# Optimization experiments

Measured on AMD Instinct MI355X. Metric: run time of the kernel, lower is better.

The kernel has to match this reference:

```python
import jax, jax.numpy as jnp
import numpy as np
from jax import lax

B, EMB, HEADS, HD, LAYERS, FIX, ADAPT, MLP, NCLS = 32, 768, 12, 64, 12, 6, 6, 3072, 100
PE_N, PE_D = 100, 256
SCALE = 1.0 / np.sqrt(HD)


def _ln(x, g, b, eps=1e-5):
    m = jnp.mean(x, axis=-1, keepdims=True)
    v = jnp.mean((x - m) ** 2, axis=-1, keepdims=True)
    return (x - m) / jnp.sqrt(v + eps) * g + b


def _vit_block(x, g1, b1, qkvw, qkvb, pw, pb, g2, b2, f1w, f1b, f2w, f2b):
    Bn, N, _ = x.shape
    h = _ln(x, g1, b1)
    qkv = (h @ qkvw + qkvb).reshape(Bn, N, 3, HEADS, HD)
    q, k, v = [qkv[:, :, i].transpose(0, 2, 1, 3) for i in range(3)]  # [B,H,N,hd]
    attn = jax.nn.softmax(jnp.einsum('bhqd,bhkd->bhqk', q, k) * SCALE, axis=-1)
    o = jnp.einsum('bhqk,bhkd->bhqd', attn, v).transpose(0, 2, 1, 3).reshape(Bn, N, EMB)
    x = x + (o @ pw + pb)
    h = _ln(x, g2, b2)
    return x + (jax.nn.gelu(h @ f1w + f1b, approximate=False) @ f2w + f2b)


def _sinusoid_table():
    pos = np.arange(PE_N)[:, None].astype(np.float64)
    j = np.arange(PE_D)[None, :]
    ang = pos / np.power(10000.0, 2 * (j // 2) / PE_D)
    tab = ang.copy()
    tab[:, 0::2] = np.sin(ang[:, 0::2])
    tab[:, 1::2] = np.cos(ang[:, 1::2])
    return jnp.asarray(tab, dtype=jnp.float32)


def setup_inputs() -> dict:
    key = jax.random.key(0)
    ks = iter(jax.random.split(key, 40))
    r = lambda shape: jax.random.normal(next(ks), shape, dtype=jnp.float32) * 0.02
    inp = {
        'x': jax.random.normal(next(ks), (B, 3, 224, 224), dtype=jnp.float32),
        'budget': jax.random.uniform(next(ks), (B,), dtype=jnp.float32),
        'pe_table': _sinusoid_table(),
        'lat_w1': r((PE_D, EMB)), 'lat_b1': r((EMB,)),
        'lat_ln_g': jnp.ones((EMB,), jnp.float32), 'lat_ln_b': jnp.zeros((EMB,), jnp.float32),
        'lat_w2': r((EMB, EMB)), 'lat_b2': r((EMB,)),
        'patch_w': r((EMB, 3, 16, 16)), 'patch_b': r((EMB,)),
        'cls_token': r((1, 1, EMB)), 'pos_embed': r((1, 198, EMB)),
        'sched_w': r((EMB, ADAPT)), 'sched_b': r((ADAPT,)),
        'ln1_g': jnp.ones((LAYERS, EMB), jnp.float32), 'ln1_b': jnp.zeros((LAYERS, EMB), jnp.float32),
        'qkv_w': r((LAYERS, EMB, 3 * EMB)), 'qkv_b': r((LAYERS, 3 * EMB)),
        'proj_w': r((LAYERS, EMB, EMB)), 'proj_b': r((LAYERS, EMB)),
        'ln2_g': jnp.ones((LAYERS, EMB), jnp.float32), 'ln2_b': jnp.zeros((LAYERS, EMB), jnp.float32),
        'fc1_w': r((LAYERS, EMB, MLP)), 'fc1_b': r((LAYERS, MLP)),
        'fc2_w': r((LAYERS, MLP, EMB)), 'fc2_b': r((LAYERS, EMB)),
        'norm_g': jnp.ones((EMB,), jnp.float32), 'norm_b': jnp.zeros((EMB,), jnp.float32),
        'head_w': r((EMB, NCLS)), 'head_b': r((NCLS,)),
    }
    return inp


def reference(x, budget, pe_table, lat_w1, lat_b1, lat_ln_g, lat_ln_b, lat_w2, lat_b2,
              patch_w, patch_b, cls_token, pos_embed, sched_w, sched_b,
              ln1_g, ln1_b, qkv_w, qkv_b, proj_w, proj_b, ln2_g, ln2_b,
              fc1_w, fc1_b, fc2_w, fc2_b, norm_g, norm_b, head_w, head_b):
    Bn = x.shape[0]
    bud = lax.stop_gradient(budget)
    # latency encoder
    idx = jnp.round(bud * (PE_N - 1)).astype(jnp.int32)
    h = pe_table[idx] @ lat_w1 + lat_b1
    h = jax.nn.gelu(h, approximate=False)
    h = _ln(h, lat_ln_g, lat_ln_b)
    lat = (h @ lat_w2 + lat_b2)[:, None, :]  # [B,1,EMB]
    # patch embed: conv16 s16 -> [B,EMB,14,14]
    p = lax.conv_general_dilated(x, patch_w, (16, 16), 'VALID',
                                 dimension_numbers=('NCHW', 'OIHW', 'NCHW'))
    p = (p + patch_b[None, :, None, None]).reshape(Bn, EMB, 196).transpose(0, 2, 1)
    tok = jnp.concatenate([lat, jnp.broadcast_to(cls_token, (Bn, 1, EMB)), p], axis=1)
    tok = tok + pos_embed  # [B,198,EMB]
    blk = lambda t, i: _vit_block(t, ln1_g[i], ln1_b[i], qkv_w[i], qkv_b[i], proj_w[i], proj_b[i],
                                  ln2_g[i], ln2_b[i], fc1_w[i], fc1_b[i], fc2_w[i], fc2_b[i])
    for i in range(FIX):
        tok = blk(tok, i)
    # layer routing (eval path): per-sample top-k over adaptive layers
    logits = tok[:, 0] @ sched_w + sched_b  # [B,ADAPT]
    k = jnp.maximum(jnp.ceil(bud * ADAPT).astype(jnp.int32), 1)  # [B]
    ranks = jnp.argsort(jnp.argsort(-logits, axis=-1), axis=-1)
    active = ranks < k[:, None]  # [B,ADAPT] bool
    t = tok[:, 1:]  # drop latency token -> [B,197,EMB]
    for i in range(ADAPT):
        out = blk(t, FIX + i)
        t = jnp.where(active[:, i, None, None], out, t)
    t = _ln(t, norm_g, norm_b)
    return t[:, 0] @ head_w + head_b
```

## Files before the change

kernel.cpp:

```cpp
#include <hip/hip_runtime.h>
#include <hip/hip_bf16.h>
#include <math.h>


using bf16   = __hip_bfloat16;
using short8 = __attribute__((ext_vector_type(8))) short;
using f32x4  = __attribute__((ext_vector_type(4))) float;

#define GLD16(gptr, lptr)                                                            \
    __builtin_amdgcn_global_load_lds((const __attribute__((address_space(1))) void*)(gptr), \
                                     (__attribute__((address_space(3))) void*)(lptr), 16, 0, 0)

__device__ __forceinline__ void split2(float x, short& h, short& l)
{
    unsigned u  = __float_as_uint(x);
    unsigned hr = (u + 0x7fffu + ((u >> 16) & 1u)) & 0xffff0000u;
    h = (short)(hr >> 16);
    float res = x - __uint_as_float(hr);
    l = (short)(__float_as_uint(res) >> 16);
}

__global__ __launch_bounds__(256) void trans_split_kernel(const float* __restrict__ W,
                                                          short* __restrict__ Wh,
                                                          short* __restrict__ Wl,
                                                          int K, int N)
{
    __shared__ float tile[32][33];
    int n0 = blockIdx.x * 32, k0 = blockIdx.y * 32;
    int c = threadIdx.x & 31, r = threadIdx.x >> 5;
    #pragma unroll
    for (int i = 0; i < 32; i += 8)
        tile[r + i][c] = W[(size_t)(k0 + r + i) * N + n0 + c];
    __syncthreads();
    #pragma unroll
    for (int i = 0; i < 32; i += 8) {
        short h, l; split2(tile[c][r + i], h, l);
        size_t o = (size_t)(n0 + r + i) * K + k0 + c;
        Wh[o] = h; Wl[o] = l;
    }
}

__global__ void split_kernel(const float* __restrict__ in, short* __restrict__ h,
                             short* __restrict__ l, int n)
{
    int i = blockIdx.x * 256 + threadIdx.x;
    if (i >= n) return;
    short hh, ll; split2(in[i], hh, ll);
    h[i] = hh; l[i] = ll;
}

__global__ void im2col_split_kernel(const float* __restrict__ x,
                                    short* __restrict__ Ah, short* __restrict__ Al)
{
    int idx = blockIdx.x * 256 + threadIdx.x;
    if (idx >= 6272 * 768) return;
    int k = idx % 768;
    int row = idx / 768;
    int b = row / 196, p = row % 196;
    int py = p / 14, px = p % 14;
    int c = k >> 8, rem = k & 255;
    int i = rem >> 4, j = rem & 15;
    float v = x[(((size_t)b * 3 + c) * 224 + py * 16 + i) * 224 + px * 16 + j];
    short h, l; split2(v, h, l);
    Ah[idx] = h; Al[idx] = l;
}

template<bool GELU, bool RES, bool SPLITOUT>
__global__ __launch_bounds__(256) void gemm3_kernel(const short* __restrict__ Ah,
                                                    const short* __restrict__ Al,
                                                    const short* __restrict__ Bh,
                                                    const short* __restrict__ Bl,
                                                    const float* __restrict__ bias,
                                                    const float* __restrict__ resid,
                                                    float* __restrict__ Cf,
                                                    short* __restrict__ Ch,
                                                    short* __restrict__ Cl,
                                                    int M, int N, int K)
{
    __shared__ __align__(16) short sm[2 * 4 * 128 * 32];
    const int tid  = threadIdx.x;
    const int lane = tid & 63;
    const int w    = tid >> 6;
    const int wm   = w >> 1, wn = w & 1;
    const int m0   = blockIdx.y * 128;
    const int n0   = blockIdx.x * 128;
    const int col  = lane & 15;
    const int quad = lane >> 4;
    const int srow = lane >> 2;
    const int skc  = (((lane & 3) ^ ((lane >> 3) & 3)) * 8);
    const int rswz = (quad ^ ((col >> 1) & 3)) * 8;

    f32x4 acc[4][4];
    #pragma unroll
    for (int i = 0; i < 4; ++i)
        #pragma unroll
        for (int j = 0; j < 4; ++j) acc[i][j] = (f32x4)0.f;

    const short* Ahb = Ah + (size_t)m0 * K;
    const short* Alb = Al + (size_t)m0 * K;
    const short* Bhb = Bh + (size_t)n0 * K;
    const short* Blb = Bl + (size_t)n0 * K;

    auto stage = [&](int buf, int t) {
        const int k0 = t << 5;
        short* dst = &sm[buf * 16384];
        #pragma unroll
        for (int i = 0; i < 2; ++i) {
            int r = w * 32 + i * 16;
            size_t go = (size_t)(r + srow) * K + k0 + skc;
            GLD16(Ahb + go, dst + r * 32);
            GLD16(Alb + go, dst + 4096 + r * 32);
            GLD16(Bhb + go, dst + 8192 + r * 32);
            GLD16(Blb + go, dst + 12288 + r * 32);
        }
    };

    auto compute = [&](int buf) {
        const short* cb = &sm[buf * 16384];
        short8 ah[4], al[4];
        #pragma unroll
        for (int mi = 0; mi < 4; ++mi) {
            int ao = (wm * 64 + mi * 16 + col) * 32 + rswz;
            ah[mi] = *(const short8*)(cb + ao);
            al[mi] = *(const short8*)(cb + 4096 + ao);
        }
        #pragma unroll
        for (int ni = 0; ni < 4; ++ni) {
            int bo = (wn * 64 + ni * 16 + col) * 32 + rswz;
            short8 bh = *(const short8*)(cb + 8192 + bo);
            short8 bl = *(const short8*)(cb + 12288 + bo);
            #pragma unroll
            for (int mi = 0; mi < 4; ++mi) {
                acc[mi][ni] = __builtin_amdgcn_mfma_f32_16x16x32_bf16(ah[mi], bh, acc[mi][ni], 0, 0, 0);
                acc[mi][ni] = __builtin_amdgcn_mfma_f32_16x16x32_bf16(al[mi], bh, acc[mi][ni], 0, 0, 0);
                acc[mi][ni] = __builtin_amdgcn_mfma_f32_16x16x32_bf16(ah[mi], bl, acc[mi][ni], 0, 0, 0);
            }
        }
    };

    const int nk = K >> 5;
    stage(0, 0);
    __syncthreads();
    int cur = 0;
    for (int t = 0; t < nk - 1; ++t) {
        stage(cur ^ 1, t + 1);
        compute(cur);
        __syncthreads();
        cur ^= 1;
    }
    compute(cur);

    #pragma unroll
    for (int mi = 0; mi < 4; ++mi) {
        #pragma unroll
        for (int ni = 0; ni < 4; ++ni) {
            int gcol = n0 + wn * 64 + ni * 16 + col;
            float bv = bias[gcol];
            #pragma unroll
            for (int r = 0; r < 4; ++r) {
                int grow = m0 + wm * 64 + mi * 16 + quad * 4 + r;
                if (grow < M) {
                    float v = acc[mi][ni][r] + bv;
                    if (RES) v += resid[(size_t)grow * N + gcol];
                    if (GELU) v = 0.5f * v * (1.f + erff(v * 0.70710678118654752f));
                    size_t o = (size_t)grow * N + gcol;
                    if (SPLITOUT) { short h, l; split2(v, h, l); Ch[o] = h; Cl[o] = l; }
                    else          Cf[o] = v;
                }
            }
        }
    }
}

__global__ __launch_bounds__(256) void ln_kernel(const float* __restrict__ x,
                                                 const float* __restrict__ g,
                                                 const float* __restrict__ bta,
                                                 short* __restrict__ outh,
                                                 short* __restrict__ outl, int M)
{
    int row = blockIdx.x * 4 + (threadIdx.x >> 6);
    int lane = threadIdx.x & 63;
    if (row >= M) return;
    const float* xr = x + (size_t)row * 768;
    float vals[12];
    float s = 0.f;
    #pragma unroll
    for (int i = 0; i < 12; ++i) { vals[i] = xr[lane + i * 64]; s += vals[i]; }
    #pragma unroll
    for (int off = 32; off; off >>= 1) s += __shfl_xor(s, off);
    float mean = s * (1.f / 768.f);
    float vs = 0.f;
    #pragma unroll
    for (int i = 0; i < 12; ++i) { float d = vals[i] - mean; vs += d * d; }
    #pragma unroll
    for (int off = 32; off; off >>= 1) vs += __shfl_xor(vs, off);
    float rstd = rsqrtf(vs * (1.f / 768.f) + 1e-5f);
    size_t rb = (size_t)row * 768;
    #pragma unroll
    for (int i = 0; i < 12; ++i) {
        int c = lane + i * 64;
        short h, l; split2((vals[i] - mean) * rstd * g[c] + bta[c], h, l);
        outh[rb + c] = h; outl[rb + c] = l;
    }
}

__global__ __launch_bounds__(256) void attn_kernel(const float* __restrict__ qkv,
                                                   short* __restrict__ Oh,
                                                   short* __restrict__ Ol, int S)
{
    __shared__ float Ks[128 * 64];
    __shared__ float Vs[128 * 64];
    int bh = blockIdx.x;
    int b = bh / 12, h = bh % 12;
    const float* base = qkv + (size_t)b * S * 2304;
    int tid = threadIdx.x;
    int r = tid;
    bool act = (r < S);
    float q[64];
    #pragma unroll
    for (int d = 0; d < 64; ++d) q[d] = 0.f;
    if (act) {
        const float4* qp = (const float4*)(base + (size_t)r * 2304 + h * 64);
        #pragma unroll
        for (int d4 = 0; d4 < 16; ++d4) {
            float4 t = qp[d4];
            q[4 * d4] = t.x; q[4 * d4 + 1] = t.y; q[4 * d4 + 2] = t.z; q[4 * d4 + 3] = t.w;
        }
    }
    float o[64];
    #pragma unroll
    for (int d = 0; d < 64; ++d) o[d] = 0.f;
    float m = -1e30f, l = 0.f;

    for (int jc = 0; jc < S; jc += 128) {
        int cnt = min(128, S - jc);
        __syncthreads();
        for (int idx = tid; idx < cnt * 64; idx += 256) {
            int j = idx >> 6, d = idx & 63;
            const float* rp = base + (size_t)(jc + j) * 2304 + h * 64 + d;
            Ks[idx] = rp[768];
            Vs[idx] = rp[1536];
        }
        __syncthreads();
        if (act) {
            for (int j = 0; j < cnt; ++j) {
                const float4* kr = (const float4*)&Ks[j * 64];
                float s0 = 0.f, s1 = 0.f, s2 = 0.f, s3 = 0.f;
                #pragma unroll
                for (int d4 = 0; d4 < 16; ++d4) {
                    float4 kv = kr[d4];
                    s0 += q[4 * d4]     * kv.x;
                    s1 += q[4 * d4 + 1] * kv.y;
                    s2 += q[4 * d4 + 2] * kv.z;
                    s3 += q[4 * d4 + 3] * kv.w;
                }
                float s = ((s0 + s1) + (s2 + s3)) * 0.125f;
                float mn = fmaxf(m, s);
                float alpha = expf(m - mn);
                float p = expf(s - mn);
                l = l * alpha + p;
                m = mn;
                const float4* vr = (const float4*)&Vs[j * 64];
                #pragma unroll
                for (int d4 = 0; d4 < 16; ++d4) {
                    float4 vv = vr[d4];
                    o[4 * d4]     = o[4 * d4]     * alpha + p * vv.x;
                    o[4 * d4 + 1] = o[4 * d4 + 1] * alpha + p * vv.y;
                    o[4 * d4 + 2] = o[4 * d4 + 2] * alpha + p * vv.z;
                    o[4 * d4 + 3] = o[4 * d4 + 3] * alpha + p * vv.w;
                }
            }
        }
    }
    if (act) {
        float inv = 1.f / l;
        size_t rb = (size_t)(b * S + r) * 768 + h * 64;
        #pragma unroll
        for (int d = 0; d < 64; ++d) {
            short hh, ll; split2(o[d] * inv, hh, ll);
            Oh[rb + d] = hh; Ol[rb + d] = ll;
        }
    }
}

__global__ __launch_bounds__(256) void latent_kernel(const float* __restrict__ pe_table,
                                                     const float* __restrict__ budget,
                                                     const float* __restrict__ w1, const float* __restrict__ b1,
                                                     const float* __restrict__ lng, const float* __restrict__ lnb,
                                                     const float* __restrict__ w2, const float* __restrict__ b2,
                                                     float* __restrict__ lat)
{
    int b = blockIdx.x, tid = threadIdx.x;
    __shared__ float pe[256];
    __shared__ float hbuf[768];
    __shared__ float red[256];
    int idx = (int)rintf(budget[b] * 99.f);
    pe[tid] = pe_table[idx * 256 + tid];
    __syncthreads();
    float hv[3];
    #pragma unroll
    for (int t = 0; t < 3; ++t) {
        int colc = tid + t * 256;
        float a = b1[colc];
        for (int k = 0; k < 256; ++k) a += pe[k] * w1[k * 768 + colc];
        hv[t] = 0.5f * a * (1.f + erff(a * 0.70710678118654752f));
    }
    float s = hv[0] + hv[1] + hv[2];
    red[tid] = s; __syncthreads();
    for (int o = 128; o > 0; o >>= 1) { if (tid < o) red[tid] += red[tid + o]; __syncthreads(); }
    float mean = red[0] * (1.f / 768.f);
    __syncthreads();
    float vs = 0.f;
    #pragma unroll
    for (int t = 0; t < 3; ++t) { float d = hv[t] - mean; vs += d * d; }
    red[tid] = vs; __syncthreads();
    for (int o = 128; o > 0; o >>= 1) { if (tid < o) red[tid] += red[tid + o]; __syncthreads(); }
    float rstd = rsqrtf(red[0] * (1.f / 768.f) + 1e-5f);
    __syncthreads();
    #pragma unroll
    for (int t = 0; t < 3; ++t) {
        int colc = tid + t * 256;
        hbuf[colc] = (hv[t] - mean) * rstd * lng[colc] + lnb[colc];
    }
    __syncthreads();
    #pragma unroll
    for (int t = 0; t < 3; ++t) {
        int colc = tid + t * 256;
        float a = b2[colc];
        for (int k = 0; k < 768; ++k) a += hbuf[k] * w2[k * 768 + colc];
        lat[b * 768 + colc] = a;
    }
}

__global__ void assemble_kernel(const float* __restrict__ lat, const float* __restrict__ cls,
                                const float* __restrict__ P, const float* __restrict__ pos,
                                float* __restrict__ T)
{
    int idx = blockIdx.x * 256 + threadIdx.x;
    if (idx >= 32 * 198 * 768) return;
    int c = idx % 768;
    int row = idx / 768;
    int b = row / 198, t = row % 198;
    float v;
    if (t == 0)      v = lat[b * 768 + c];
    else if (t == 1) v = cls[c];
    else             v = P[((size_t)b * 196 + (t - 2)) * 768 + c];
    T[idx] = v + pos[t * 768 + c];
}

__global__ void sched_kernel(const float* __restrict__ T, const float* __restrict__ sw,
                             const float* __restrict__ sb, const float* __restrict__ budget,
                             int* __restrict__ active)
{
    int b = blockIdx.x, lane = threadIdx.x;
    const float* xr = T + (size_t)b * 198 * 768;
    float acc[6] = {0, 0, 0, 0, 0, 0};
    for (int k = lane; k < 768; k += 64) {
        float xv = xr[k];
        #pragma unroll
        for (int i = 0; i < 6; ++i) acc[i] += xv * sw[k * 6 + i];
    }
    #pragma unroll
    for (int i = 0; i < 6; ++i)
        #pragma unroll
        for (int off = 32; off; off >>= 1) acc[i] += __shfl_xor(acc[i], off);
    if (lane == 0) {
        float lg[6];
        #pragma unroll
        for (int i = 0; i < 6; ++i) lg[i] = acc[i] + sb[i];
        int k = (int)ceilf(budget[b] * 6.f);
        if (k < 1) k = 1;
        for (int i = 0; i < 6; ++i) {
            int rank = 0;
            for (int j = 0; j < 6; ++j)
                rank += (lg[j] > lg[i]) || (lg[j] == lg[i] && j < i);
            active[b * 6 + i] = (rank < k) ? 1 : 0;
        }
    }
}

__global__ void droplat_kernel(const float* __restrict__ T, float* __restrict__ T2)
{
    int idx = blockIdx.x * 256 + threadIdx.x;
    if (idx >= 32 * 197 * 768) return;
    int c = idx % 768;
    int row = idx / 768;
    int b = row / 197, t = row % 197;
    T2[idx] = T[((size_t)b * 198 + t + 1) * 768 + c];
}

__global__ void select_kernel(float* __restrict__ T2, const float* __restrict__ OUT,
                              const int* __restrict__ active, int layer)
{
    int idx = blockIdx.x * 256 + threadIdx.x;
    if (idx >= 32 * 197 * 768) return;
    int b = idx / (197 * 768);
    if (active[b * 6 + layer]) T2[idx] = OUT[idx];
}

__global__ __launch_bounds__(128) void head_kernel(const float* __restrict__ T2,
                                                   const float* __restrict__ g,
                                                   const float* __restrict__ bta,
                                                   const float* __restrict__ hw,
                                                   const float* __restrict__ hb,
                                                   float* __restrict__ out)
{
    int b = blockIdx.x, tid = threadIdx.x;
    __shared__ float hn[768];
    __shared__ float red[128];
    const float* xr = T2 + (size_t)b * 197 * 768;
    float v[6];
    float s = 0.f;
    #pragma unroll
    for (int i = 0; i < 6; ++i) { v[i] = xr[tid + i * 128]; s += v[i]; }
    red[tid] = s; __syncthreads();
    for (int o = 64; o > 0; o >>= 1) { if (tid < o) red[tid] += red[tid + o]; __syncthreads(); }
    float mean = red[0] * (1.f / 768.f);
    __syncthreads();
    float vs = 0.f;
    #pragma unroll
    for (int i = 0; i < 6; ++i) { float d = v[i] - mean; vs += d * d; }
    red[tid] = vs; __syncthreads();
    for (int o = 64; o > 0; o >>= 1) { if (tid < o) red[tid] += red[tid + o]; __syncthreads(); }
    float rstd = rsqrtf(red[0] * (1.f / 768.f) + 1e-5f);
    #pragma unroll
    for (int i = 0; i < 6; ++i) {
        int c = tid + i * 128;
        hn[c] = (v[i] - mean) * rstd * g[c] + bta[c];
    }
    __syncthreads();
    if (tid < 100) {
        float a = hb[tid];
        for (int k = 0; k < 768; ++k) a += hn[k] * hw[k * 100 + tid];
        out[b * 100 + tid] = a;
    }
}

extern "C" void kernel_launch(void* const* d_in, const int* in_sizes, int n_in,
                              void* d_out, int out_size, void* d_ws, size_t ws_size,
                              hipStream_t stream)
{
    const float* x        = (const float*)d_in[0];
    const float* budget   = (const float*)d_in[1];
    const float* pe_table = (const float*)d_in[2];
    const float* lat_w1   = (const float*)d_in[3];
    const float* lat_b1   = (const float*)d_in[4];
    const float* lat_ln_g = (const float*)d_in[5];
    const float* lat_ln_b = (const float*)d_in[6];
    const float* lat_w2   = (const float*)d_in[7];
    const float* lat_b2   = (const float*)d_in[8];
    const float* patch_w  = (const float*)d_in[9];
    const float* patch_b  = (const float*)d_in[10];
    const float* cls_tok  = (const float*)d_in[11];
    const float* pos_emb  = (const float*)d_in[12];
    const float* sched_w  = (const float*)d_in[13];
    const float* sched_b  = (const float*)d_in[14];
    const float* ln1_g    = (const float*)d_in[15];
    const float* ln1_b    = (const float*)d_in[16];
    const float* qkv_w    = (const float*)d_in[17];
    const float* qkv_b    = (const float*)d_in[18];
    const float* proj_w   = (const float*)d_in[19];
    const float* proj_b   = (const float*)d_in[20];
    const float* ln2_g    = (const float*)d_in[21];
    const float* ln2_b    = (const float*)d_in[22];
    const float* fc1_w    = (const float*)d_in[23];
    const float* fc1_b    = (const float*)d_in[24];
    const float* fc2_w    = (const float*)d_in[25];
    const float* fc2_b    = (const float*)d_in[26];
    const float* norm_g   = (const float*)d_in[27];
    const float* norm_b   = (const float*)d_in[28];
    const float* head_w   = (const float*)d_in[29];
    const float* head_b   = (const float*)d_in[30];
    float* out = (float*)d_out;
    (void)in_sizes; (void)n_in; (void)out_size; (void)ws_size;

    char* ws = (char*)d_ws;
    size_t off = 0;
    auto alloc = [&](size_t bytes) -> char* {
        char* p = ws + off;
        off = (off + bytes + 255) & ~(size_t)255;
        return p;
    };
    short* sQKVh = (short*)alloc(2304ull * 768 * 2);
    short* sQKVl = (short*)alloc(2304ull * 768 * 2);
    short* sPRJh = (short*)alloc(768ull * 768 * 2);
    short* sPRJl = (short*)alloc(768ull * 768 * 2);
    short* sFC1h = (short*)alloc(3072ull * 768 * 2);
    short* sFC1l = (short*)alloc(3072ull * 768 * 2);
    short* sFC2h = (short*)alloc(768ull * 3072 * 2);
    short* sFC2l = (short*)alloc(768ull * 3072 * 2);
    short* pwh   = (short*)alloc(768ull * 768 * 2);
    short* pwl   = (short*)alloc(768ull * 768 * 2);
    float* T     = (float*)alloc(6400ull * 768 * 4);
    float* T2    = (float*)alloc(6400ull * 768 * 4);
    float* OUT   = (float*)alloc(6400ull * 768 * 4);
    short* Hh    = (short*)alloc(6400ull * 768 * 2);
    short* Hl    = (short*)alloc(6400ull * 768 * 2);
    float* QKV   = (float*)alloc(6336ull * 2304 * 4);
    short* Oh    = (short*)alloc(6400ull * 768 * 2);
    short* Ol    = (short*)alloc(6400ull * 768 * 2);
    short* Mh    = (short*)alloc(6400ull * 3072 * 2);
    short* Ml    = (short*)alloc(6400ull * 3072 * 2);
    float* lat   = (float*)alloc(32ull * 768 * 4);
    int*   act   = (int*)alloc(32 * 6 * 4);
    float* P     = QKV;
    short* Aph   = Mh;
    short* Apl   = Ml;

    im2col_split_kernel<<<(6272 * 768 + 255) / 256, 256, 0, stream>>>(x, Aph, Apl);
    split_kernel<<<(768 * 768 + 255) / 256, 256, 0, stream>>>(patch_w, pwh, pwl, 768 * 768);
    latent_kernel<<<32, 256, 0, stream>>>(pe_table, budget, lat_w1, lat_b1,
                                          lat_ln_g, lat_ln_b, lat_w2, lat_b2, lat);
    gemm3_kernel<false, false, false><<<dim3(6, 49), 256, 0, stream>>>(
        Aph, Apl, pwh, pwl, patch_b, nullptr, P, nullptr, nullptr, 6272, 768, 768);
    assemble_kernel<<<(32 * 198 * 768 + 255) / 256, 256, 0, stream>>>(lat, cls_tok, P, pos_emb, T);

    for (int l = 0; l < 6; ++l) {
        trans_split_kernel<<<dim3(72, 24), 256, 0, stream>>>(qkv_w + (size_t)l * 768 * 2304, sQKVh, sQKVl, 768, 2304);
        trans_split_kernel<<<dim3(24, 24), 256, 0, stream>>>(proj_w + (size_t)l * 768 * 768, sPRJh, sPRJl, 768, 768);
        trans_split_kernel<<<dim3(96, 24), 256, 0, stream>>>(fc1_w + (size_t)l * 768 * 3072, sFC1h, sFC1l, 768, 3072);
        trans_split_kernel<<<dim3(24, 96), 256, 0, stream>>>(fc2_w + (size_t)l * 3072 * 768, sFC2h, sFC2l, 3072, 768);

        ln_kernel<<<6336 / 4, 256, 0, stream>>>(T, ln1_g + l * 768, ln1_b + l * 768, Hh, Hl, 6336);
        gemm3_kernel<false, false, false><<<dim3(18, 50), 256, 0, stream>>>(
            Hh, Hl, sQKVh, sQKVl, qkv_b + l * 2304, nullptr, QKV, nullptr, nullptr, 6336, 2304, 768);
        attn_kernel<<<384, 256, 0, stream>>>(QKV, Oh, Ol, 198);
        gemm3_kernel<false, true, false><<<dim3(6, 50), 256, 0, stream>>>(
            Oh, Ol, sPRJh, sPRJl, proj_b + l * 768, T, T, nullptr, nullptr, 6336, 768, 768);
        ln_kernel<<<6336 / 4, 256, 0, stream>>>(T, ln2_g + l * 768, ln2_b + l * 768, Hh, Hl, 6336);
        gemm3_kernel<true, false, true><<<dim3(24, 50), 256, 0, stream>>>(
            Hh, Hl, sFC1h, sFC1l, fc1_b + l * 3072, nullptr, nullptr, Mh, Ml, 6336, 3072, 768);
        gemm3_kernel<false, true, false><<<dim3(6, 50), 256, 0, stream>>>(
            Mh, Ml, sFC2h, sFC2l, fc2_b + l * 768, T, T, nullptr, nullptr, 6336, 768, 3072);
    }

    sched_kernel<<<32, 64, 0, stream>>>(T, sched_w, sched_b, budget, act);
    droplat_kernel<<<(32 * 197 * 768 + 255) / 256, 256, 0, stream>>>(T, T2);

    for (int i = 0; i < 6; ++i) {
        int l = 6 + i;
        trans_split_kernel<<<dim3(72, 24), 256, 0, stream>>>(qkv_w + (size_t)l * 768 * 2304, sQKVh, sQKVl, 768, 2304);
        trans_split_kernel<<<dim3(24, 24), 256, 0, stream>>>(proj_w + (size_t)l * 768 * 768, sPRJh, sPRJl, 768, 768);
        trans_split_kernel<<<dim3(96, 24), 256, 0, stream>>>(fc1_w + (size_t)l * 768 * 3072, sFC1h, sFC1l, 768, 3072);
        trans_split_kernel<<<dim3(24, 96), 256, 0, stream>>>(fc2_w + (size_t)l * 3072 * 768, sFC2h, sFC2l, 3072, 768);

        ln_kernel<<<6304 / 4, 256, 0, stream>>>(T2, ln1_g + l * 768, ln1_b + l * 768, Hh, Hl, 6304);
        gemm3_kernel<false, false, false><<<dim3(18, 50), 256, 0, stream>>>(
            Hh, Hl, sQKVh, sQKVl, qkv_b + l * 2304, nullptr, QKV, nullptr, nullptr, 6304, 2304, 768);
        attn_kernel<<<384, 256, 0, stream>>>(QKV, Oh, Ol, 197);
        gemm3_kernel<false, true, false><<<dim3(6, 50), 256, 0, stream>>>(
            Oh, Ol, sPRJh, sPRJl, proj_b + l * 768, T2, OUT, nullptr, nullptr, 6304, 768, 768);
        ln_kernel<<<6304 / 4, 256, 0, stream>>>(OUT, ln2_g + l * 768, ln2_b + l * 768, Hh, Hl, 6304);
        gemm3_kernel<true, false, true><<<dim3(24, 50), 256, 0, stream>>>(
            Hh, Hl, sFC1h, sFC1l, fc1_b + l * 3072, nullptr, nullptr, Mh, Ml, 6304, 3072, 768);
        gemm3_kernel<false, true, false><<<dim3(6, 50), 256, 0, stream>>>(
            Mh, Ml, sFC2h, sFC2l, fc2_b + l * 768, OUT, OUT, nullptr, nullptr, 6304, 768, 3072);
        select_kernel<<<(32 * 197 * 768 + 255) / 256, 256, 0, stream>>>(T2, OUT, act, i);
    }

    head_kernel<<<32, 128, 0, stream>>>(T2, norm_g, norm_b, head_w, head_b, out);
}
```

Before: 7.758 ms.

## Split attention queries across two blocks and use lazy softmax rescaling

Each (batch, head) attention block is split into two 128-thread blocks that each handle half the query rows. This doubles the grid to 768 blocks so more CUs stay busy, and halves the idle threads in the 256-wide blocks where only 198 rows were active. K/V tiles shrink to 64 rows and are loaded with float4, and the online softmax only rescales the accumulator when some lane's score exceeds the running max by more than 8. This skips most per-key alpha multiplies and uses fast __expf. The trade-off is that K/V are loaded twice per head, plus a warp-vote branch and slightly looser numerics.

```diff
diff --git a/kernel.cpp b/kernel.cpp
--- a/kernel.cpp
+++ b/kernel.cpp
@@ -204,18 +204,22 @@
     }
 }
 
-__global__ __launch_bounds__(256) void attn_kernel(const float* __restrict__ qkv,
+__global__ __launch_bounds__(128) void attn_kernel(const float* __restrict__ qkv,
                                                    short* __restrict__ Oh,
                                                    short* __restrict__ Ol, int S)
 {
-    __shared__ float Ks[128 * 64];
-    __shared__ float Vs[128 * 64];
-    int bh = blockIdx.x;
+    __shared__ float Ks[64 * 64];
+    __shared__ float Vs[64 * 64];
+    int blk  = blockIdx.x;
+    int bh   = blk >> 1, half = blk & 1;
     int b = bh / 12, h = bh % 12;
+    int halfRows = (S + 1) >> 1;
+    int q0   = half * halfRows;
+    int qcnt = min(halfRows, S - q0);
     const float* base = qkv + (size_t)b * S * 2304;
     int tid = threadIdx.x;
-    int r = tid;
-    bool act = (r < S);
+    int r = q0 + tid;
+    bool act = (tid < qcnt);
     float q[64];
     #pragma unroll
     for (int d = 0; d < 64; ++d) q[d] = 0.f;
@@ -232,14 +236,14 @@
     for (int d = 0; d < 64; ++d) o[d] = 0.f;
     float m = -1e30f, l = 0.f;
 
-    for (int jc = 0; jc < S; jc += 128) {
-        int cnt = min(128, S - jc);
+    for (int jc = 0; jc < S; jc += 64) {
+        int cnt = min(64, S - jc);
         __syncthreads();
-        for (int idx = tid; idx < cnt * 64; idx += 256) {
-            int j = idx >> 6, d = idx & 63;
-            const float* rp = base + (size_t)(jc + j) * 2304 + h * 64 + d;
-            Ks[idx] = rp[768];
-            Vs[idx] = rp[1536];
+        for (int idx = tid; idx < cnt * 16; idx += 128) {
+            int j = idx >> 4, d4 = idx & 15;
+            const float4* rp = (const float4*)(base + (size_t)(jc + j) * 2304 + h * 64) + d4;
+            ((float4*)Ks)[j * 16 + d4] = rp[192];
+            ((float4*)Vs)[j * 16 + d4] = rp[384];
         }
         __syncthreads();
         if (act) {
@@ -255,19 +259,24 @@
                     s3 += q[4 * d4 + 3] * kv.w;
                 }
                 float s = ((s0 + s1) + (s2 + s3)) * 0.125f;
-                float mn = fmaxf(m, s);
-                float alpha = expf(m - mn);
-                float p = expf(s - mn);
-                l = l * alpha + p;
-                m = mn;
+                if (!__all(s <= m + 8.f)) {
+                    float mn = fmaxf(m, s);
+                    float alpha = __expf(m - mn);
+                    l *= alpha;
+                    #pragma unroll
+                    for (int d = 0; d < 64; ++d) o[d] *= alpha;
+                    m = mn;
+                }
+                float p = __expf(s - m);
+                l += p;
                 const float4* vr = (const float4*)&Vs[j * 64];
                 #pragma unroll
                 for (int d4 = 0; d4 < 16; ++d4) {
                     float4 vv = vr[d4];
-                    o[4 * d4]     = o[4 * d4]     * alpha + p * vv.x;
-                    o[4 * d4 + 1] = o[4 * d4 + 1] * alpha + p * vv.y;
-                    o[4 * d4 + 2] = o[4 * d4 + 2] * alpha + p * vv.z;
-                    o[4 * d4 + 3] = o[4 * d4 + 3] * alpha + p * vv.w;
+                    o[4 * d4]     += p * vv.x;
+                    o[4 * d4 + 1] += p * vv.y;
+                    o[4 * d4 + 2] += p * vv.z;
+                    o[4 * d4 + 3] += p * vv.w;
                 }
             }
         }
@@ -524,7 +533,7 @@
         ln_kernel<<<6336 / 4, 256, 0, stream>>>(T, ln1_g + l * 768, ln1_b + l * 768, Hh, Hl, 6336);
         gemm3_kernel<false, false, false><<<dim3(18, 50), 256, 0, stream>>>(
             Hh, Hl, sQKVh, sQKVl, qkv_b + l * 2304, nullptr, QKV, nullptr, nullptr, 6336, 2304, 768);
-        attn_kernel<<<384, 256, 0, stream>>>(QKV, Oh, Ol, 198);
+        attn_kernel<<<768, 128, 0, stream>>>(QKV, Oh, Ol, 198);
         gemm3_kernel<false, true, false><<<dim3(6, 50), 256, 0, stream>>>(
             Oh, Ol, sPRJh, sPRJl, proj_b + l * 768, T, T, nullptr, nullptr, 6336, 768, 768);
         ln_kernel<<<6336 / 4, 256, 0, stream>>>(T, ln2_g + l * 768, ln2_b + l * 768, Hh, Hl, 6336);
@@ -547,7 +556,7 @@
         ln_kernel<<<6304 / 4, 256, 0, stream>>>(T2, ln1_g + l * 768, ln1_b + l * 768, Hh, Hl, 6304);
         gemm3_kernel<false, false, false><<<dim3(18, 50), 256, 0, stream>>>(
             Hh, Hl, sQKVh, sQKVl, qkv_b + l * 2304, nullptr, QKV, nullptr, nullptr, 6304, 2304, 768);
-        attn_kernel<<<384, 256, 0, stream>>>(QKV, Oh, Ol, 197);
+        attn_kernel<<<768, 128, 0, stream>>>(QKV, Oh, Ol, 197);
         gemm3_kernel<false, true, false><<<dim3(6, 50), 256, 0, stream>>>(
             Oh, Ol, sPRJh, sPRJl, proj_b + l * 768, T2, OUT, nullptr, nullptr, 6304, 768, 768);
         ln_kernel<<<6304 / 4, 256, 0, stream>>>(OUT, ln2_g + l * 768, ln2_b + l * 768, Hh, Hl, 6304);
```

After: 7.651 ms. About the same (-1.4%).
